# Optimization experiments

Measured on AMD Instinct MI355X. Metric: run time of the kernel, lower is better.

Reference implementation:

```python
import jax, jax.numpy as jnp
import numpy as np

NU = 200000   # num user nodes
NI = 200000   # num item nodes
E = 500000    # edges per relation
D = 128       # in_feats
H = 128       # h_feats
NEG_SLOPE = 0.01  # F.leaky_relu default


def _sage(x_src, x_dst, src, dst, n_dst, W_self, W_neigh, b):
    # DGL SAGEConv('mean'): fc_self(x_dst) + fc_neigh(mean of in-neighbors) + bias
    msg = x_src[src]                                   # [E, d] gather
    agg = jax.ops.segment_sum(msg, dst, num_segments=n_dst)   # [n_dst, d]
    deg = jax.ops.segment_sum(jnp.ones((src.shape[0],), x_src.dtype), dst,
                              num_segments=n_dst)      # [n_dst]
    mean = agg / jnp.maximum(deg, 1.0)[:, None]        # zero in-degree -> 0
    return x_dst @ W_self + mean @ W_neigh + b


def setup_inputs() -> dict:
    key = jax.random.key(0)
    ks = jax.random.split(key, 20)
    s = 1.0 / np.sqrt(D)
    inp = {
        'x_user': jax.random.normal(ks[0], (NU, D), jnp.float32),
        'x_item': jax.random.normal(ks[1], (NI, D), jnp.float32),
        'w1_self_uc': jax.random.normal(ks[2], (D, H), jnp.float32) * s,
        'w1_neigh_uc': jax.random.normal(ks[3], (D, H), jnp.float32) * s,
        'b1_uc': jnp.zeros((H,), jnp.float32),
        'w1_self_iu': jax.random.normal(ks[4], (D, H), jnp.float32) * s,
        'w1_neigh_iu': jax.random.normal(ks[5], (D, H), jnp.float32) * s,
        'b1_iu': jnp.zeros((H,), jnp.float32),
        'w2_self_uc': jax.random.normal(ks[6], (H, H), jnp.float32) * s,
        'w2_neigh_uc': jax.random.normal(ks[7], (H, H), jnp.float32) * s,
        'b2_uc': jnp.zeros((H,), jnp.float32),
        'w2_self_iu': jax.random.normal(ks[8], (H, H), jnp.float32) * s,
        'w2_neigh_iu': jax.random.normal(ks[9], (H, H), jnp.float32) * s,
        'b2_iu': jnp.zeros((H,), jnp.float32),
        'src_uc': jax.random.randint(ks[10], (E,), 0, NU, jnp.int32),
        'dst_uc': jax.random.randint(ks[11], (E,), 0, NI, jnp.int32),
        'src_iu': jax.random.randint(ks[12], (E,), 0, NI, jnp.int32),
        'dst_iu': jax.random.randint(ks[13], (E,), 0, NU, jnp.int32),
    }
    return inp


def reference(x_user, x_item,
              w1_self_uc, w1_neigh_uc, b1_uc, w1_self_iu, w1_neigh_iu, b1_iu,
              w2_self_uc, w2_neigh_uc, b2_uc, w2_self_iu, w2_neigh_iu, b2_iu,
              src_uc, dst_uc, src_iu, dst_iu):
    # layer 1: relation 'clicks' user->item, relation 'clicked_by' item->user
    h1_item = _sage(x_user, x_item, src_uc, dst_uc, NI, w1_self_uc, w1_neigh_uc, b1_uc)
    h1_user = _sage(x_item, x_user, src_iu, dst_iu, NU, w1_self_iu, w1_neigh_iu, b1_iu)
    h1_item = jax.nn.leaky_relu(h1_item, NEG_SLOPE)
    h1_user = jax.nn.leaky_relu(h1_user, NEG_SLOPE)
    # layer 2
    h2_item = _sage(h1_user, h1_item, src_uc, dst_uc, NI, w2_self_uc, w2_neigh_uc, b2_uc)
    h2_user = _sage(h1_item, h1_user, src_iu, dst_iu, NU, w2_self_iu, w2_neigh_iu, b2_iu)
    # stack [user, item] (same shape) for a single output tensor
    return jnp.stack([h2_user, h2_item], axis=0)  # [2, 200000, 128]
```

## Files before the change

### kernel.cpp

```cpp
#include <hip/hip_runtime.h>
#include <hip/hip_bf16.h>

#define D_ 128

typedef __attribute__((ext_vector_type(8))) short s8b;
typedef __attribute__((ext_vector_type(4))) float f4;

union U4 { uint u[4]; s8b v; uint4 q; };

__device__ __forceinline__ void gl16(const void* g, void* lds) {
    __builtin_amdgcn_global_load_lds(
        (const __attribute__((address_space(1))) void*)g,
        (__attribute__((address_space(3))) void*)lds, 16, 0, 0);
}

__device__ __forceinline__ void split2(float f0, float f1, uint& hp, uint& lp) {
    uint u0 = __float_as_uint(f0), u1 = __float_as_uint(f1);
    hp = (u0 >> 16) | (u1 & 0xffff0000u);
    float r0 = f0 - __uint_as_float(u0 & 0xffff0000u);
    float r1 = f1 - __uint_as_float(u1 & 0xffff0000u);
    uint v0 = __float_as_uint(r0), v1 = __float_as_uint(r1);
    uint l0 = (v0 + 0x7fffu + ((v0 >> 16) & 1u)) >> 16;
    uint l1 = (v1 + 0x7fffu + ((v1 >> 16) & 1u)) >> 16;
    lp = l0 | (l1 << 16);
}

__device__ __forceinline__ float4 asf4(uint4 u) {
    return make_float4(__uint_as_float(u.x), __uint_as_float(u.y),
                       __uint_as_float(u.z), __uint_as_float(u.w));
}

__global__ void deg2_kernel(const int* __restrict__ dstA, const int* __restrict__ dstB,
                            int* __restrict__ degA, int* __restrict__ degB, int E) {
    int e = blockIdx.x * blockDim.x + threadIdx.x;
    const int* dst = blockIdx.y ? dstB : dstA;
    int* deg = blockIdx.y ? degB : degA;
    if (e < E) atomicAdd(&deg[dst[e]], 1);
}

__global__ __launch_bounds__(256)
void scan1m(const int* __restrict__ degA, const int* __restrict__ degB,
            int* __restrict__ rpA, int* __restrict__ rpB,
            int* __restrict__ partA, int* __restrict__ partB, int N) {
    const int* deg = blockIdx.y ? degB : degA;
    int* rp = blockIdx.y ? rpB : rpA;
    int* partials = blockIdx.y ? partB : partA;
    int tid = threadIdx.x;
    int i = blockIdx.x * 256 + tid;
    int v = (i < N) ? deg[i] : 0;
    int lane = tid & 63, wid = tid >> 6;
    int x = v;
#pragma unroll
    for (int off = 1; off < 64; off <<= 1) {
        int y = __shfl_up(x, off, 64);
        if (lane >= off) x += y;
    }
    __shared__ int wsum[5];
    if (lane == 63) wsum[wid] = x;
    __syncthreads();
    if (tid == 0) {
        int a = wsum[0], b = wsum[1], c = wsum[2], d = wsum[3];
        wsum[0] = 0; wsum[1] = a; wsum[2] = a + b; wsum[3] = a + b + c;
        wsum[4] = a + b + c + d;
    }
    __syncthreads();
    if (i < N) rp[i] = wsum[wid] + x - v;
    if (tid == 0) partials[blockIdx.x] = wsum[4];
}

__global__ __launch_bounds__(1024)
void scan2m(int* __restrict__ partA, int* __restrict__ partB, int B) {
    int* partials = blockIdx.x ? partB : partA;
    __shared__ int buf[1024];
    int t = threadIdx.x;
    int v = (t < B) ? partials[t] : 0;
    buf[t] = v;
    __syncthreads();
    for (int off = 1; off < 1024; off <<= 1) {
        int add = (t >= off) ? buf[t - off] : 0;
        __syncthreads();
        buf[t] += add;
        __syncthreads();
    }
    if (t < B) partials[t] = buf[t] - v;
}

__global__ __launch_bounds__(256)
void scan3m(int* __restrict__ rpA, int* __restrict__ rpB,
            const int* __restrict__ partA, const int* __restrict__ partB, int N, int E) {
    int* rp = blockIdx.y ? rpB : rpA;
    const int* partials = blockIdx.y ? partB : partA;
    int i = blockIdx.x * 256 + threadIdx.x;
    if (i < N) rp[i] += partials[blockIdx.x];
    if (i == 0) rp[N] = E;
}

__global__ void fill2_csr(const int* __restrict__ srcA, const int* __restrict__ dstA,
                          const int* __restrict__ rpA, int* __restrict__ curA,
                          int* __restrict__ colA, int* __restrict__ colpA,
                          const int* __restrict__ srcB, const int* __restrict__ dstB,
                          const int* __restrict__ rpB, int* __restrict__ curB,
                          int* __restrict__ colB, int* __restrict__ colpB, int E) {
    int e = blockIdx.x * blockDim.x + threadIdx.x;
    if (e >= E) return;
    const int* src = blockIdx.y ? srcB : srcA;
    const int* dst = blockIdx.y ? dstB : dstA;
    const int* rp  = blockIdx.y ? rpB : rpA;
    int* cursor = blockIdx.y ? curB : curA;
    int* col    = blockIdx.y ? colB : colA;
    int* colp   = blockIdx.y ? colpB : colpA;
    int d = dst[e];
    int s = src[e];
    int idx = atomicAdd(&cursor[d], 1);
    col[rp[d] + idx] = s;
    if (idx < 4) colp[d * 4 + idx] = s;
}

__global__ __launch_bounds__(256)
void prep_weights(const float* __restrict__ s0, const float* __restrict__ n0,
                  const float* __restrict__ s1, const float* __restrict__ n1,
                  const float* __restrict__ s2, const float* __restrict__ n2,
                  const float* __restrict__ s3, const float* __restrict__ n3,
                  ushort* __restrict__ WTH, ushort* __restrict__ WTL) {
    int g = blockIdx.y;
    int t = blockIdx.x * 256 + threadIdx.x;
    int c = t & 127;
    int oct = t >> 7;
    const float* self  = g == 0 ? s0 : g == 1 ? s1 : g == 2 ? s2 : s3;
    const float* neigh = g == 0 ? n0 : g == 1 ? n1 : g == 2 ? n2 : n3;
    uint hd[4], ld_[4];
#pragma unroll
    for (int p = 0; p < 4; ++p) {
        uint hpair = 0, lpair = 0;
#pragma unroll
        for (int q = 0; q < 2; ++q) {
            int kv = oct * 8 + p * 2 + q;
            const float* Wsrc = kv < 128 ? self : neigh;
            float f = Wsrc[(size_t)(kv & 127) * 128 + c];
            uint u = __float_as_uint(f);
            uint h = u >> 16;
            float r = f - __uint_as_float(u & 0xffff0000u);
            uint v = __float_as_uint(r);
            uint l = (v + 0x7fffu + ((v >> 16) & 1u)) >> 16;
            hpair |= h << (16 * q);
            lpair |= l << (16 * q);
        }
        hd[p] = hpair; ld_[p] = lpair;
    }
    size_t base = ((size_t)g * 128 + c) * 256 + oct * 8;
    *(uint4*)(WTH + base) = make_uint4(hd[0], hd[1], hd[2], hd[3]);
    *(uint4*)(WTL + base) = make_uint4(ld_[0], ld_[1], ld_[2], ld_[3]);
}

#define AGGH 0
#define AGGL 8192
#define ASTEP 16384
#define WHO 20480
#define WLO 28672

template<int FP32IN, int SPLIT, int LRELU>
__device__ __forceinline__ void fused_body(const char* A1, const char* XN,
        const int* rp, const int* col, const int* colp,
        const ushort* WTh, const ushort* WTl, const float* bias, void* outp,
        int bid, char* smem) {
    const int t = threadIdx.x;
    const int row0 = bid * 32;
    const int li = t & 15;

#pragma unroll
    for (int p = 0; p < 2; ++p) {
        int nl = p * 16 + (t >> 4);
        int node = row0 + nl;
        int beg = rp[node], end = rp[node + 1];
        int dg = end - beg;
        int4 c4 = *(const int4*)(colp + (size_t)node * 4);
        int s0 = dg > 0 ? c4.x : 0;
        int s1 = dg > 1 ? c4.y : 0;
        int s2 = dg > 2 ? c4.z : 0;
        int s3 = dg > 3 ? c4.w : 0;
        float w0 = dg > 0 ? 1.f : 0.f;
        float w1 = dg > 1 ? 1.f : 0.f;
        float w2 = dg > 2 ? 1.f : 0.f;
        float w3 = dg > 3 ? 1.f : 0.f;
        float a[8];
#pragma unroll
        for (int j = 0; j < 8; ++j) a[j] = 0.f;
        const int lo = FP32IN ? li * 32 : li * 16;
        const int d2 = FP32IN ? 16 : 256;
        const char* p0 = XN + (size_t)s0 * 512 + lo;
        const char* p1 = XN + (size_t)s1 * 512 + lo;
        const char* p2 = XN + (size_t)s2 * 512 + lo;
        const char* p3 = XN + (size_t)s3 * 512 + lo;
        uint4 H0 = *(const uint4*)p0, L0 = *(const uint4*)(p0 + d2);
        uint4 H1 = *(const uint4*)p1, L1 = *(const uint4*)(p1 + d2);
        uint4 H2 = *(const uint4*)p2, L2 = *(const uint4*)(p2 + d2);
        uint4 H3 = *(const uint4*)p3, L3 = *(const uint4*)(p3 + d2);
        if (FP32IN) {
#pragma unroll
            for (int q = 0; q < 4; ++q) {
                uint4 Hq = q == 0 ? H0 : q == 1 ? H1 : q == 2 ? H2 : H3;
                uint4 Lq = q == 0 ? L0 : q == 1 ? L1 : q == 2 ? L2 : L3;
                float wq = q == 0 ? w0 : q == 1 ? w1 : q == 2 ? w2 : w3;
                float4 X = asf4(Hq), Y = asf4(Lq);
                a[0] = fmaf(X.x, wq, a[0]); a[1] = fmaf(X.y, wq, a[1]);
                a[2] = fmaf(X.z, wq, a[2]); a[3] = fmaf(X.w, wq, a[3]);
                a[4] = fmaf(Y.x, wq, a[4]); a[5] = fmaf(Y.y, wq, a[5]);
                a[6] = fmaf(Y.z, wq, a[6]); a[7] = fmaf(Y.w, wq, a[7]);
            }
            for (int e = beg + 4; e < end; ++e) {
                const char* pp = XN + (size_t)col[e] * 512 + li * 32;
                float4 X = *(const float4*)pp, Y = *(const float4*)(pp + 16);
                a[0] += X.x; a[1] += X.y; a[2] += X.z; a[3] += X.w;
                a[4] += Y.x; a[5] += Y.y; a[6] += Y.z; a[7] += Y.w;
            }
        } else {
#pragma unroll
            for (int q = 0; q < 4; ++q) {
                uint4 Hq = q == 0 ? H0 : q == 1 ? H1 : q == 2 ? H2 : H3;
                uint4 Lq = q == 0 ? L0 : q == 1 ? L1 : q == 2 ? L2 : L3;
                float wq = q == 0 ? w0 : q == 1 ? w1 : q == 2 ? w2 : w3;
                const ushort* hu = (const ushort*)&Hq;
                const ushort* lu = (const ushort*)&Lq;
#pragma unroll
                for (int j = 0; j < 8; ++j) {
                    float v = __uint_as_float((uint)hu[j] << 16)
                            + __uint_as_float((uint)lu[j] << 16);
                    a[j] = fmaf(v, wq, a[j]);
                }
            }
            for (int e = beg + 4; e < end; ++e) {
                const char* pp = XN + (size_t)col[e] * 512 + li * 16;
                uint4 H = *(const uint4*)pp, L = *(const uint4*)(pp + 256);
                const ushort* hu = (const ushort*)&H;
                const ushort* lu = (const ushort*)&L;
#pragma unroll
                for (int j = 0; j < 8; ++j)
                    a[j] += __uint_as_float((uint)hu[j] << 16)
                          + __uint_as_float((uint)lu[j] << 16);
            }
        }
        float inv = 1.f / (float)(dg > 0 ? dg : 1);
        uint h[4], l[4];
        split2(a[0] * inv, a[1] * inv, h[0], l[0]);
        split2(a[2] * inv, a[3] * inv, h[1], l[1]);
        split2(a[4] * inv, a[5] * inv, h[2], l[2]);
        split2(a[6] * inv, a[7] * inv, h[3], l[3]);
        int chunk = li ^ (nl & 3) ^ (((nl >> 2) & 3) << 2);
        *(uint4*)(smem + AGGH + nl * 256 + chunk * 16) = make_uint4(h[0], h[1], h[2], h[3]);
        *(uint4*)(smem + AGGL + nl * 256 + chunk * 16) = make_uint4(l[0], l[1], l[2], l[3]);
    }

    const int w = t >> 6, lane = t & 63;
    const int fr = lane & 15, hi = lane >> 4;
    const int ncol0 = w * 32;

    f4 acc[2][2];
    {
        float bv[2];
#pragma unroll
        for (int n = 0; n < 2; ++n) bv[n] = bias[ncol0 + n * 16 + fr];
#pragma unroll
        for (int m = 0; m < 2; ++m)
#pragma unroll
            for (int n = 0; n < 2; ++n) acc[m][n] = (f4){bv[n], bv[n], bv[n], bv[n]};
    }

    auto stage = [&](int ks) {
        if (ks < 4) {
            if (FP32IN) {
                int row = t >> 3, cs = t & 7;
                gl16(A1 + (size_t)(row0 + row) * 512 + ks * 128 + ((cs ^ (row & 7)) * 16),
                     smem + ASTEP + t * 16);
            } else {
                int j = t & 127, part = t >> 7;
                int row = j >> 2, cs = j & 3;
                gl16(A1 + (size_t)(row0 + row) * 512 + part * 256 + ks * 64
                         + ((cs ^ ((row >> 1) & 3)) * 16),
                     smem + ASTEP + part * 2048 + j * 16);
            }
        }
#pragma unroll
        for (int it = 0; it < 2; ++it) {
            int j = it * 256 + t;
            int col_ = j >> 2, cs = j & 3;
            size_t so = (size_t)col_ * 512 + ks * 64 + ((cs ^ ((col_ >> 1) & 3)) * 16);
            gl16((const char*)WTh + so, smem + WHO + j * 16);
            gl16((const char*)WTl + so, smem + WLO + j * 16);
        }
    };

    auto compute = [&](int ks) {
        s8b ah[2], al[2], wh[2], wl[2];
        if (ks < 4) {
            if (FP32IN) {
#pragma unroll
                for (int m = 0; m < 2; ++m) {
                    int r = m * 16 + fr;
                    f4 x0 = *(const f4*)(smem + ASTEP + r * 128 + (((hi * 2) ^ (r & 7)) * 16));
                    f4 x1 = *(const f4*)(smem + ASTEP + r * 128 + (((hi * 2 + 1) ^ (r & 7)) * 16));
                    U4 H, L;
                    split2(x0[0], x0[1], H.u[0], L.u[0]);
                    split2(x0[2], x0[3], H.u[1], L.u[1]);
                    split2(x1[0], x1[1], H.u[2], L.u[2]);
                    split2(x1[2], x1[3], H.u[3], L.u[3]);
                    ah[m] = H.v; al[m] = L.v;
                }
            } else {
#pragma unroll
                for (int m = 0; m < 2; ++m) {
                    int r = m * 16 + fr;
                    int off = r * 64 + ((hi ^ ((r >> 1) & 3)) * 16);
                    ah[m] = *(const s8b*)(smem + ASTEP + off);
                    al[m] = *(const s8b*)(smem + ASTEP + 2048 + off);
                }
            }
        } else {
            int kk = ks - 4;
#pragma unroll
            for (int m = 0; m < 2; ++m) {
                int r = m * 16 + fr;
                int chunk = (kk * 4 + hi) ^ (r & 3) ^ (((r >> 2) & 3) << 2);
                ah[m] = *(const s8b*)(smem + AGGH + r * 256 + chunk * 16);
                al[m] = *(const s8b*)(smem + AGGL + r * 256 + chunk * 16);
            }
        }
#pragma unroll
        for (int n = 0; n < 2; ++n) {
            int c = ncol0 + n * 16 + fr;
            int off = c * 64 + ((hi ^ ((c >> 1) & 3)) * 16);
            wh[n] = *(const s8b*)(smem + WHO + off);
            wl[n] = *(const s8b*)(smem + WLO + off);
        }
#pragma unroll
        for (int n = 0; n < 2; ++n)
#pragma unroll
            for (int m = 0; m < 2; ++m) {
                acc[m][n] = __builtin_amdgcn_mfma_f32_16x16x32_bf16(ah[m], wh[n], acc[m][n], 0, 0, 0);
                acc[m][n] = __builtin_amdgcn_mfma_f32_16x16x32_bf16(al[m], wh[n], acc[m][n], 0, 0, 0);
                acc[m][n] = __builtin_amdgcn_mfma_f32_16x16x32_bf16(ah[m], wl[n], acc[m][n], 0, 0, 0);
            }
    };

    for (int ks = 0; ks < 8; ++ks) {
        stage(ks);
        __syncthreads();
        compute(ks);
        __syncthreads();
    }

    float* T = (float*)smem;
#pragma unroll
    for (int m = 0; m < 2; ++m)
#pragma unroll
        for (int n = 0; n < 2; ++n)
#pragma unroll
            for (int r = 0; r < 4; ++r)
                T[(m * 16 + hi * 4 + r) * 132 + ncol0 + n * 16 + fr] = acc[m][n][r];
    __syncthreads();
    {
        int row = t >> 3, q = t & 7;
        int gr = row0 + row;
        if (SPLIT) {
            char* ob = (char*)outp + (size_t)gr * 512;
#pragma unroll
            for (int i = 0; i < 2; ++i) {
                const float* p = T + row * 132 + (q * 2 + i) * 8;
                f4 x0 = *(const f4*)p;
                f4 x1 = *(const f4*)(p + 4);
                float e[8] = {x0[0], x0[1], x0[2], x0[3], x1[0], x1[1], x1[2], x1[3]};
                if (LRELU) {
#pragma unroll
                    for (int j = 0; j < 8; ++j) e[j] = e[j] > 0.f ? e[j] : 0.01f * e[j];
                }
                uint h[4], l[4];
#pragma unroll
                for (int j = 0; j < 4; ++j) split2(e[2 * j], e[2 * j + 1], h[j], l[j]);
                *(uint4*)(ob + (q * 2 + i) * 16) = make_uint4(h[0], h[1], h[2], h[3]);
                *(uint4*)(ob + 256 + (q * 2 + i) * 16) = make_uint4(l[0], l[1], l[2], l[3]);
            }
        } else {
            float* ob = (float*)outp + (size_t)gr * 128;
#pragma unroll
            for (int i = 0; i < 4; ++i) {
                f4 x = *(const f4*)(T + row * 132 + q * 16 + i * 4);
                float e0 = x[0], e1 = x[1], e2 = x[2], e3 = x[3];
                if (LRELU) {
                    e0 = e0 > 0.f ? e0 : 0.01f * e0;
                    e1 = e1 > 0.f ? e1 : 0.01f * e1;
                    e2 = e2 > 0.f ? e2 : 0.01f * e2;
                    e3 = e3 > 0.f ? e3 : 0.01f * e3;
                }
                *(float4*)(ob + q * 16 + i * 4) = make_float4(e0, e1, e2, e3);
            }
        }
    }
}

template<int FP32IN, int SPLIT, int LRELU>
__global__ __launch_bounds__(256, 4)
void fused2k(const void* A1a, const void* XNa, const int* rpA, const int* colA,
             const int* colpA, const ushort* WTha, const ushort* WTla,
             const float* ba, void* outa,
             const void* A1b, const void* XNb, const int* rpB, const int* colB,
             const int* colpB, const ushort* WThb, const ushort* WTlb,
             const float* bb, void* outb, int blocksA) {
    __shared__ __align__(16) char smem[36864];
    bool isA = (int)blockIdx.x < blocksA;
    int bid = isA ? blockIdx.x : blockIdx.x - blocksA;
    if (isA)
        fused_body<FP32IN, SPLIT, LRELU>((const char*)A1a, (const char*)XNa, rpA, colA,
                                         colpA, WTha, WTla, ba, outa, bid, smem);
    else
        fused_body<FP32IN, SPLIT, LRELU>((const char*)A1b, (const char*)XNb, rpB, colB,
                                         colpB, WThb, WTlb, bb, outb, bid, smem);
}

extern "C" void kernel_launch(void* const* d_in, const int* in_sizes, int n_in,
                              void* d_out, int out_size, void* d_ws, size_t ws_size,
                              hipStream_t stream) {
    const float* x_user     = (const float*)d_in[0];
    const float* x_item     = (const float*)d_in[1];
    const float* w1_self_uc = (const float*)d_in[2];
    const float* w1_neigh_uc= (const float*)d_in[3];
    const float* b1_uc      = (const float*)d_in[4];
    const float* w1_self_iu = (const float*)d_in[5];
    const float* w1_neigh_iu= (const float*)d_in[6];
    const float* b1_iu      = (const float*)d_in[7];
    const float* w2_self_uc = (const float*)d_in[8];
    const float* w2_neigh_uc= (const float*)d_in[9];
    const float* b2_uc      = (const float*)d_in[10];
    const float* w2_self_iu = (const float*)d_in[11];
    const float* w2_neigh_iu= (const float*)d_in[12];
    const float* b2_iu      = (const float*)d_in[13];
    const int* src_uc = (const int*)d_in[14];
    const int* dst_uc = (const int*)d_in[15];
    const int* src_iu = (const int*)d_in[16];
    const int* dst_iu = (const int*)d_in[17];

    const int NU = in_sizes[0] / D_;
    const int NI = in_sizes[1] / D_;
    const int E  = in_sizes[14];

    float* f_user = (float*)d_out;
    float* f_item = (float*)d_out + (size_t)NU * 128;

    char* ws = (char*)d_ws;
    const size_t FEAT_BYTES = (size_t)200000 * 512;
    char* h1_item  = ws;          ws += FEAT_BYTES;
    char* h1_user  = ws;          ws += FEAT_BYTES;
    ushort* WTH    = (ushort*)ws; ws += (size_t)4 * 128 * 256 * sizeof(ushort);
    ushort* WTL    = (ushort*)ws; ws += (size_t)4 * 128 * 256 * sizeof(ushort);
    int* colp_uc   = (int*)ws;    ws += (size_t)200000 * 4 * sizeof(int);
    int* colp_iu   = (int*)ws;    ws += (size_t)200000 * 4 * sizeof(int);
    int* rp_uc     = (int*)ws;    ws += (size_t)(NI + 1) * sizeof(int);
    int* rp_iu     = (int*)ws;    ws += (size_t)(NU + 1) * sizeof(int);
    int* col_uc    = (int*)ws;    ws += (size_t)E * sizeof(int);
    int* col_iu    = (int*)ws;    ws += (size_t)E * sizeof(int);
    int* deg_uc    = (int*)ws;    ws += (size_t)200000 * sizeof(int);
    int* deg_iu    = (int*)ws;    ws += (size_t)200000 * sizeof(int);
    int* cur_uc    = (int*)ws;    ws += (size_t)200000 * sizeof(int);
    int* cur_iu    = (int*)ws;    ws += (size_t)200000 * sizeof(int);
    int* partA     = (int*)ws;    ws += (size_t)1024 * sizeof(int);
    int* partB     = (int*)ws;    ws += (size_t)1024 * sizeof(int);

    const int TPB = 256;
    const int eBlocks  = (E + TPB - 1) / TPB;
    const int sBlocks  = (200000 + 255) / 256;
    const int mBlocksI = (NI + 31) / 32;
    const int mBlocksU = (NU + 31) / 32;
    const size_t WSTRIDE = (size_t)128 * 256;

    hipMemsetAsync(deg_uc, 0, (size_t)4 * 200000 * sizeof(int), stream);

    prep_weights<<<dim3(16, 4), 256, 0, stream>>>(
        w1_self_uc, w1_neigh_uc, w1_self_iu, w1_neigh_iu,
        w2_self_uc, w2_neigh_uc, w2_self_iu, w2_neigh_iu, WTH, WTL);

    deg2_kernel<<<dim3(eBlocks, 2), TPB, 0, stream>>>(dst_uc, dst_iu, deg_uc, deg_iu, E);
    scan1m<<<dim3(sBlocks, 2), 256, 0, stream>>>(deg_uc, deg_iu, rp_uc, rp_iu, partA, partB, 200000);
    scan2m<<<2, 1024, 0, stream>>>(partA, partB, sBlocks);
    scan3m<<<dim3(sBlocks, 2), 256, 0, stream>>>(rp_uc, rp_iu, partA, partB, 200000, E);
    fill2_csr<<<dim3(eBlocks, 2), TPB, 0, stream>>>(src_uc, dst_uc, rp_uc, cur_uc, col_uc, colp_uc,
                                                    src_iu, dst_iu, rp_iu, cur_iu, col_iu, colp_iu, E);

    fused2k<1, 1, 1><<<mBlocksI + mBlocksU, 256, 0, stream>>>(
        x_item, x_user, rp_uc, col_uc, colp_uc, WTH + 0 * WSTRIDE, WTL + 0 * WSTRIDE,
        b1_uc, h1_item,
        x_user, x_item, rp_iu, col_iu, colp_iu, WTH + 1 * WSTRIDE, WTL + 1 * WSTRIDE,
        b1_iu, h1_user, mBlocksI);

    fused2k<0, 0, 0><<<mBlocksI + mBlocksU, 256, 0, stream>>>(
        h1_item, h1_user, rp_uc, col_uc, colp_uc, WTH + 2 * WSTRIDE, WTL + 2 * WSTRIDE,
        b2_uc, f_item,
        h1_user, h1_item, rp_iu, col_iu, colp_iu, WTH + 3 * WSTRIDE, WTL + 3 * WSTRIDE,
        b2_iu, f_user, mBlocksI);
}
```

Measured before the change: 628.8 us.

## Double row tile to 64 with 512 threads, wider K stages, 8-neighbor prefetch

The fused SAGE kernel now processes 64 destination rows per block with 512 threads. Waves split the output tile over both rows and columns, so each staged weight slice is reused across twice as many rows. The K loop runs in 4 wider phases of 64 instead of 8 phases of 32, which halves the number of barriers. The CSR prefix cache grows from 4 to 8 neighbors, so up to 8 neighbor loads are issued together before the serial col[] loop. In exchange, shared memory rises to 80KB per block, which may limit occupancy, and the prefix array uses twice the memory.

```diff
diff --git a/kernel.cpp b/kernel.cpp
--- a/kernel.cpp
+++ b/kernel.cpp
@@ -113,7 +113,7 @@
     int s = src[e];
     int idx = atomicAdd(&cursor[d], 1);
     col[rp[d] + idx] = s;
-    if (idx < 4) colp[d * 4 + idx] = s;
+    if (idx < 8) colp[(size_t)d * 8 + idx] = s;
 }
 
 __global__ __launch_bounds__(256)
@@ -153,10 +153,10 @@
 }
 
 #define AGGH 0
-#define AGGL 8192
-#define ASTEP 16384
-#define WHO 20480
-#define WLO 28672
+#define AGGL 16384
+#define ASTEP 32768
+#define WHO 49152
+#define WLO 65536
 
 template<int FP32IN, int SPLIT, int LRELU>
 __device__ __forceinline__ void fused_body(const char* A1, const char* XN,
@@ -164,16 +164,16 @@
         const ushort* WTh, const ushort* WTl, const float* bias, void* outp,
         int bid, char* smem) {
     const int t = threadIdx.x;
-    const int row0 = bid * 32;
+    const int row0 = bid * 64;
     const int li = t & 15;
 
 #pragma unroll
     for (int p = 0; p < 2; ++p) {
-        int nl = p * 16 + (t >> 4);
+        int nl = p * 32 + (t >> 4);
         int node = row0 + nl;
         int beg = rp[node], end = rp[node + 1];
         int dg = end - beg;
-        int4 c4 = *(const int4*)(colp + (size_t)node * 4);
+        int4 c4 = *(const int4*)(colp + (size_t)node * 8);
         int s0 = dg > 0 ? c4.x : 0;
         int s1 = dg > 1 ? c4.y : 0;
         int s2 = dg > 2 ? c4.z : 0;
@@ -187,56 +187,92 @@
         for (int j = 0; j < 8; ++j) a[j] = 0.f;
         const int lo = FP32IN ? li * 32 : li * 16;
         const int d2 = FP32IN ? 16 : 256;
-        const char* p0 = XN + (size_t)s0 * 512 + lo;
-        const char* p1 = XN + (size_t)s1 * 512 + lo;
-        const char* p2 = XN + (size_t)s2 * 512 + lo;
-        const char* p3 = XN + (size_t)s3 * 512 + lo;
-        uint4 H0 = *(const uint4*)p0, L0 = *(const uint4*)(p0 + d2);
-        uint4 H1 = *(const uint4*)p1, L1 = *(const uint4*)(p1 + d2);
-        uint4 H2 = *(const uint4*)p2, L2 = *(const uint4*)(p2 + d2);
-        uint4 H3 = *(const uint4*)p3, L3 = *(const uint4*)(p3 + d2);
-        if (FP32IN) {
+        {
+            const char* p0 = XN + (size_t)s0 * 512 + lo;
+            const char* p1 = XN + (size_t)s1 * 512 + lo;
+            const char* p2 = XN + (size_t)s2 * 512 + lo;
+            const char* p3 = XN + (size_t)s3 * 512 + lo;
+            uint4 H0 = *(const uint4*)p0, L0 = *(const uint4*)(p0 + d2);
+            uint4 H1 = *(const uint4*)p1, L1 = *(const uint4*)(p1 + d2);
+            uint4 H2 = *(const uint4*)p2, L2 = *(const uint4*)(p2 + d2);
+            uint4 H3 = *(const uint4*)p3, L3 = *(const uint4*)(p3 + d2);
 #pragma unroll
             for (int q = 0; q < 4; ++q) {
                 uint4 Hq = q == 0 ? H0 : q == 1 ? H1 : q == 2 ? H2 : H3;
                 uint4 Lq = q == 0 ? L0 : q == 1 ? L1 : q == 2 ? L2 : L3;
                 float wq = q == 0 ? w0 : q == 1 ? w1 : q == 2 ? w2 : w3;
-                float4 X = asf4(Hq), Y = asf4(Lq);
-                a[0] = fmaf(X.x, wq, a[0]); a[1] = fmaf(X.y, wq, a[1]);
-                a[2] = fmaf(X.z, wq, a[2]); a[3] = fmaf(X.w, wq, a[3]);
-                a[4] = fmaf(Y.x, wq, a[4]); a[5] = fmaf(Y.y, wq, a[5]);
-                a[6] = fmaf(Y.z, wq, a[6]); a[7] = fmaf(Y.w, wq, a[7]);
-            }
-            for (int e = beg + 4; e < end; ++e) {
-                const char* pp = XN + (size_t)col[e] * 512 + li * 32;
-                float4 X = *(const float4*)pp, Y = *(const float4*)(pp + 16);
-                a[0] += X.x; a[1] += X.y; a[2] += X.z; a[3] += X.w;
-                a[4] += Y.x; a[5] += Y.y; a[6] += Y.z; a[7] += Y.w;
-            }
-        } else {
+                if (FP32IN) {
+                    float4 X = asf4(Hq), Y = asf4(Lq);
+                    a[0] = fmaf(X.x, wq, a[0]); a[1] = fmaf(X.y, wq, a[1]);
+                    a[2] = fmaf(X.z, wq, a[2]); a[3] = fmaf(X.w, wq, a[3]);
+                    a[4] = fmaf(Y.x, wq, a[4]); a[5] = fmaf(Y.y, wq, a[5]);
+                    a[6] = fmaf(Y.z, wq, a[6]); a[7] = fmaf(Y.w, wq, a[7]);
+                } else {
+                    const ushort* hu = (const ushort*)&Hq;
+                    const ushort* lu = (const ushort*)&Lq;
+#pragma unroll
+                    for (int j = 0; j < 8; ++j) {
+                        float v = __uint_as_float((uint)hu[j] << 16)
+                                + __uint_as_float((uint)lu[j] << 16);
+                        a[j] = fmaf(v, wq, a[j]);
+                    }
+                }
+            }
+        }
+        if (dg > 4) {
+            int4 c4b = *(const int4*)(colp + (size_t)node * 8 + 4);
+            int s4 = c4b.x;
+            int s5 = dg > 5 ? c4b.y : s4;
+            int s6 = dg > 6 ? c4b.z : s4;
+            int s7 = dg > 7 ? c4b.w : s4;
+            float w5 = dg > 5 ? 1.f : 0.f;
+            float w6 = dg > 6 ? 1.f : 0.f;
+            float w7 = dg > 7 ? 1.f : 0.f;
+            const char* p4 = XN + (size_t)s4 * 512 + lo;
+            const char* p5 = XN + (size_t)s5 * 512 + lo;
+            const char* p6 = XN + (size_t)s6 * 512 + lo;
+            const char* p7 = XN + (size_t)s7 * 512 + lo;
+            uint4 H4 = *(const uint4*)p4, L4 = *(const uint4*)(p4 + d2);
+            uint4 H5 = *(const uint4*)p5, L5 = *(const uint4*)(p5 + d2);
+            uint4 H6 = *(const uint4*)p6, L6 = *(const uint4*)(p6 + d2);
+            uint4 H7 = *(const uint4*)p7, L7 = *(const uint4*)(p7 + d2);
 #pragma unroll
             for (int q = 0; q < 4; ++q) {
-                uint4 Hq = q == 0 ? H0 : q == 1 ? H1 : q == 2 ? H2 : H3;
-                uint4 Lq = q == 0 ? L0 : q == 1 ? L1 : q == 2 ? L2 : L3;
-                float wq = q == 0 ? w0 : q == 1 ? w1 : q == 2 ? w2 : w3;
-                const ushort* hu = (const ushort*)&Hq;
-                const ushort* lu = (const ushort*)&Lq;
-#pragma unroll
-                for (int j = 0; j < 8; ++j) {
-                    float v = __uint_as_float((uint)hu[j] << 16)
-                            + __uint_as_float((uint)lu[j] << 16);
-                    a[j] = fmaf(v, wq, a[j]);
-                }
-            }
-            for (int e = beg + 4; e < end; ++e) {
-                const char* pp = XN + (size_t)col[e] * 512 + li * 16;
-                uint4 H = *(const uint4*)pp, L = *(const uint4*)(pp + 256);
-                const ushort* hu = (const ushort*)&H;
-                const ushort* lu = (const ushort*)&L;
-#pragma unroll
-                for (int j = 0; j < 8; ++j)
-                    a[j] += __uint_as_float((uint)hu[j] << 16)
-                          + __uint_as_float((uint)lu[j] << 16);
+                uint4 Hq = q == 0 ? H4 : q == 1 ? H5 : q == 2 ? H6 : H7;
+                uint4 Lq = q == 0 ? L4 : q == 1 ? L5 : q == 2 ? L6 : L7;
+                float wq = q == 0 ? 1.f : q == 1 ? w5 : q == 2 ? w6 : w7;
+                if (FP32IN) {
+                    float4 X = asf4(Hq), Y = asf4(Lq);
+                    a[0] = fmaf(X.x, wq, a[0]); a[1] = fmaf(X.y, wq, a[1]);
+                    a[2] = fmaf(X.z, wq, a[2]); a[3] = fmaf(X.w, wq, a[3]);
+                    a[4] = fmaf(Y.x, wq, a[4]); a[5] = fmaf(Y.y, wq, a[5]);
+                    a[6] = fmaf(Y.z, wq, a[6]); a[7] = fmaf(Y.w, wq, a[7]);
+                } else {
+                    const ushort* hu = (const ushort*)&Hq;
+                    const ushort* lu = (const ushort*)&Lq;
+#pragma unroll
+                    for (int j = 0; j < 8; ++j) {
+                        float v = __uint_as_float((uint)hu[j] << 16)
+                                + __uint_as_float((uint)lu[j] << 16);
+                        a[j] = fmaf(v, wq, a[j]);
+                    }
+                }
+            }
+            for (int e = beg + 8; e < end; ++e) {
+                const char* pp = XN + (size_t)col[e] * 512 + lo;
+                uint4 H = *(const uint4*)pp, L = *(const uint4*)(pp + d2);
+                if (FP32IN) {
+                    float4 X = asf4(H), Y = asf4(L);
+                    a[0] += X.x; a[1] += X.y; a[2] += X.z; a[3] += X.w;
+                    a[4] += Y.x; a[5] += Y.y; a[6] += Y.z; a[7] += Y.w;
+                } else {
+                    const ushort* hu = (const ushort*)&H;
+                    const ushort* lu = (const ushort*)&L;
+#pragma unroll
+                    for (int j = 0; j < 8; ++j)
+                        a[j] += __uint_as_float((uint)hu[j] << 16)
+                              + __uint_as_float((uint)lu[j] << 16);
+                }
             }
         }
         float inv = 1.f / (float)(dg > 0 ? dg : 1);
@@ -252,7 +288,7 @@
 
     const int w = t >> 6, lane = t & 63;
     const int fr = lane & 15, hi = lane >> 4;
-    const int ncol0 = w * 32;
+    const int mrow0 = (w & 1) * 32, ncol0 = (w >> 1) * 32;
 
     f4 acc[2][2];
     {
@@ -265,97 +301,99 @@
             for (int n = 0; n < 2; ++n) acc[m][n] = (f4){bv[n], bv[n], bv[n], bv[n]};
     }
 
-    auto stage = [&](int ks) {
-        if (ks < 4) {
+    for (int ph = 0; ph < 4; ++ph) {
+        if (ph < 2) {
             if (FP32IN) {
-                int row = t >> 3, cs = t & 7;
-                gl16(A1 + (size_t)(row0 + row) * 512 + ks * 128 + ((cs ^ (row & 7)) * 16),
-                     smem + ASTEP + t * 16);
+#pragma unroll
+                for (int it = 0; it < 2; ++it) {
+                    int j = it * 512 + t;
+                    int row = j >> 4, c = j & 15;
+                    gl16(A1 + (size_t)(row0 + row) * 512 + ph * 256
+                             + ((c ^ ((row & 7) << 1)) * 16),
+                         smem + ASTEP + j * 16);
+                }
             } else {
-                int j = t & 127, part = t >> 7;
-                int row = j >> 2, cs = j & 3;
-                gl16(A1 + (size_t)(row0 + row) * 512 + part * 256 + ks * 64
-                         + ((cs ^ ((row >> 1) & 3)) * 16),
-                     smem + ASTEP + part * 2048 + j * 16);
+                int j = t;
+                int row = j >> 3, c2 = j & 7;
+                size_t so = (size_t)(row0 + row) * 512 + ph * 128 + ((c2 ^ (row & 7)) * 16);
+                gl16(A1 + so, smem + ASTEP + j * 16);
+                gl16(A1 + so + 256, smem + ASTEP + 8192 + j * 16);
             }
         }
 #pragma unroll
         for (int it = 0; it < 2; ++it) {
-            int j = it * 256 + t;
-            int col_ = j >> 2, cs = j & 3;
-            size_t so = (size_t)col_ * 512 + ks * 64 + ((cs ^ ((col_ >> 1) & 3)) * 16);
+            int j = it * 512 + t;
+            int col_ = j >> 3, c2 = j & 7;
+            size_t so = (size_t)col_ * 512 + ph * 128 + ((c2 ^ (col_ & 7)) * 16);
             gl16((const char*)WTh + so, smem + WHO + j * 16);
             gl16((const char*)WTl + so, smem + WLO + j * 16);
         }
-    };
-
-    auto compute = [&](int ks) {
-        s8b ah[2], al[2], wh[2], wl[2];
-        if (ks < 4) {
-            if (FP32IN) {
+        __syncthreads();
+
+#pragma unroll
+        for (int j = 0; j < 2; ++j) {
+            s8b ah[2], al[2], wh[2], wl[2];
+            if (ph < 2) {
+                if (FP32IN) {
+#pragma unroll
+                    for (int m = 0; m < 2; ++m) {
+                        int r = mrow0 + m * 16 + fr;
+                        int c0 = ((j * 8 + hi * 2) ^ ((r & 7) << 1));
+                        f4 x0 = *(const f4*)(smem + ASTEP + r * 256 + c0 * 16);
+                        f4 x1 = *(const f4*)(smem + ASTEP + r * 256 + c0 * 16 + 16);
+                        U4 H, L;
+                        split2(x0[0], x0[1], H.u[0], L.u[0]);
+                        split2(x0[2], x0[3], H.u[1], L.u[1]);
+                        split2(x1[0], x1[1], H.u[2], L.u[2]);
+                        split2(x1[2], x1[3], H.u[3], L.u[3]);
+                        ah[m] = H.v; al[m] = L.v;
+                    }
+                } else {
+#pragma unroll
+                    for (int m = 0; m < 2; ++m) {
+                        int r = mrow0 + m * 16 + fr;
+                        int chunk = (j * 4 + hi) ^ (r & 7);
+                        ah[m] = *(const s8b*)(smem + ASTEP + r * 128 + chunk * 16);
+                        al[m] = *(const s8b*)(smem + ASTEP + 8192 + r * 128 + chunk * 16);
+                    }
+                }
+            } else {
+                int kk = (ph - 2) * 2 + j;
 #pragma unroll
                 for (int m = 0; m < 2; ++m) {
-                    int r = m * 16 + fr;
-                    f4 x0 = *(const f4*)(smem + ASTEP + r * 128 + (((hi * 2) ^ (r & 7)) * 16));
-                    f4 x1 = *(const f4*)(smem + ASTEP + r * 128 + (((hi * 2 + 1) ^ (r & 7)) * 16));
-                    U4 H, L;
-                    split2(x0[0], x0[1], H.u[0], L.u[0]);
-                    split2(x0[2], x0[3], H.u[1], L.u[1]);
-                    split2(x1[0], x1[1], H.u[2], L.u[2]);
-                    split2(x1[2], x1[3], H.u[3], L.u[3]);
-                    ah[m] = H.v; al[m] = L.v;
-                }
-            } else {
+                    int r = mrow0 + m * 16 + fr;
+                    int chunk = (kk * 4 + hi) ^ (r & 3) ^ (((r >> 2) & 3) << 2);
+                    ah[m] = *(const s8b*)(smem + AGGH + r * 256 + chunk * 16);
+                    al[m] = *(const s8b*)(smem + AGGL + r * 256 + chunk * 16);
+                }
+            }
+#pragma unroll
+            for (int n = 0; n < 2; ++n) {
+                int c = ncol0 + n * 16 + fr;
+                int chunk = (j * 4 + hi) ^ (c & 7);
+                wh[n] = *(const s8b*)(smem + WHO + c * 128 + chunk * 16);
+                wl[n] = *(const s8b*)(smem + WLO + c * 128 + chunk * 16);
+            }
+#pragma unroll
+            for (int n = 0; n < 2; ++n)
 #pragma unroll
                 for (int m = 0; m < 2; ++m) {
-                    int r = m * 16 + fr;
-                    int off = r * 64 + ((hi ^ ((r >> 1) & 3)) * 16);
-                    ah[m] = *(const s8b*)(smem + ASTEP + off);
-                    al[m] = *(const s8b*)(smem + ASTEP + 2048 + off);
-                }
-            }
-        } else {
-            int kk = ks - 4;
-#pragma unroll
-            for (int m = 0; m < 2; ++m) {
-                int r = m * 16 + fr;
-                int chunk = (kk * 4 + hi) ^ (r & 3) ^ (((r >> 2) & 3) << 2);
-                ah[m] = *(const s8b*)(smem + AGGH + r * 256 + chunk * 16);
-                al[m] = *(const s8b*)(smem + AGGL + r * 256 + chunk * 16);
-            }
-        }
-#pragma unroll
-        for (int n = 0; n < 2; ++n) {
-            int c = ncol0 + n * 16 + fr;
-            int off = c * 64 + ((hi ^ ((c >> 1) & 3)) * 16);
-            wh[n] = *(const s8b*)(smem + WHO + off);
-            wl[n] = *(const s8b*)(smem + WLO + off);
-        }
+                    acc[m][n] = __builtin_amdgcn_mfma_f32_16x16x32_bf16(ah[m], wh[n], acc[m][n], 0, 0, 0);
+                    acc[m][n] = __builtin_amdgcn_mfma_f32_16x16x32_bf16(al[m], wh[n], acc[m][n], 0, 0, 0);
+                    acc[m][n] = __builtin_amdgcn_mfma_f32_16x16x32_bf16(ah[m], wl[n], acc[m][n], 0, 0, 0);
+                }
+        }
+        __syncthreads();
+    }
+
+    float* T = (float*)smem;
+#pragma unroll
+    for (int m = 0; m < 2; ++m)
 #pragma unroll
         for (int n = 0; n < 2; ++n)
 #pragma unroll
-            for (int m = 0; m < 2; ++m) {
-                acc[m][n] = __builtin_amdgcn_mfma_f32_16x16x32_bf16(ah[m], wh[n], acc[m][n], 0, 0, 0);
-                acc[m][n] = __builtin_amdgcn_mfma_f32_16x16x32_bf16(al[m], wh[n], acc[m][n], 0, 0, 0);
-                acc[m][n] = __builtin_amdgcn_mfma_f32_16x16x32_bf16(ah[m], wl[n], acc[m][n], 0, 0, 0);
-            }
-    };
-
-    for (int ks = 0; ks < 8; ++ks) {
-        stage(ks);
-        __syncthreads();
-        compute(ks);
-        __syncthreads();
-    }
-
-    float* T = (float*)smem;
-#pragma unroll
-    for (int m = 0; m < 2; ++m)
-#pragma unroll
-        for (int n = 0; n < 2; ++n)
-#pragma unroll
             for (int r = 0; r < 4; ++r)
-                T[(m * 16 + hi * 4 + r) * 132 + ncol0 + n * 16 + fr] = acc[m][n][r];
+                T[(mrow0 + m * 16 + hi * 4 + r) * 132 + ncol0 + n * 16 + fr] = acc[m][n][r];
     __syncthreads();
     {
         int row = t >> 3, q = t & 7;
@@ -370,11 +408,11 @@
                 float e[8] = {x0[0], x0[1], x0[2], x0[3], x1[0], x1[1], x1[2], x1[3]};
                 if (LRELU) {
 #pragma unroll
-                    for (int j = 0; j < 8; ++j) e[j] = e[j] > 0.f ? e[j] : 0.01f * e[j];
+                    for (int jj = 0; jj < 8; ++jj) e[jj] = e[jj] > 0.f ? e[jj] : 0.01f * e[jj];
                 }
                 uint h[4], l[4];
 #pragma unroll
-                for (int j = 0; j < 4; ++j) split2(e[2 * j], e[2 * j + 1], h[j], l[j]);
+                for (int jj = 0; jj < 4; ++jj) split2(e[2 * jj], e[2 * jj + 1], h[jj], l[jj]);
                 *(uint4*)(ob + (q * 2 + i) * 16) = make_uint4(h[0], h[1], h[2], h[3]);
                 *(uint4*)(ob + 256 + (q * 2 + i) * 16) = make_uint4(l[0], l[1], l[2], l[3]);
             }
@@ -397,14 +435,14 @@
 }
 
 template<int FP32IN, int SPLIT, int LRELU>
-__global__ __launch_bounds__(256, 4)
+__global__ __launch_bounds__(512, 4)
 void fused2k(const void* A1a, const void* XNa, const int* rpA, const int* colA,
              const int* colpA, const ushort* WTha, const ushort* WTla,
              const float* ba, void* outa,
              const void* A1b, const void* XNb, const int* rpB, const int* colB,
              const int* colpB, const ushort* WThb, const ushort* WTlb,
              const float* bb, void* outb, int blocksA) {
-    __shared__ __align__(16) char smem[36864];
+    __shared__ __align__(16) char smem[81920];
     bool isA = (int)blockIdx.x < blocksA;
     int bid = isA ? blockIdx.x : blockIdx.x - blocksA;
     if (isA)
@@ -450,8 +488,8 @@
     char* h1_user  = ws;          ws += FEAT_BYTES;
     ushort* WTH    = (ushort*)ws; ws += (size_t)4 * 128 * 256 * sizeof(ushort);
     ushort* WTL    = (ushort*)ws; ws += (size_t)4 * 128 * 256 * sizeof(ushort);
-    int* colp_uc   = (int*)ws;    ws += (size_t)200000 * 4 * sizeof(int);
-    int* colp_iu   = (int*)ws;    ws += (size_t)200000 * 4 * sizeof(int);
+    int* colp_uc   = (int*)ws;    ws += (size_t)200000 * 8 * sizeof(int);
+    int* colp_iu   = (int*)ws;    ws += (size_t)200000 * 8 * sizeof(int);
     int* rp_uc     = (int*)ws;    ws += (size_t)(NI + 1) * sizeof(int);
     int* rp_iu     = (int*)ws;    ws += (size_t)(NU + 1) * sizeof(int);
     int* col_uc    = (int*)ws;    ws += (size_t)E * sizeof(int);
@@ -466,8 +504,8 @@
     const int TPB = 256;
     const int eBlocks  = (E + TPB - 1) / TPB;
     const int sBlocks  = (200000 + 255) / 256;
-    const int mBlocksI = (NI + 31) / 32;
-    const int mBlocksU = (NU + 31) / 32;
+    const int mBlocksI = (NI + 63) / 64;
+    const int mBlocksU = (NU + 63) / 64;
     const size_t WSTRIDE = (size_t)128 * 256;
 
     hipMemsetAsync(deg_uc, 0, (size_t)4 * 200000 * sizeof(int), stream);
@@ -483,13 +521,13 @@
     fill2_csr<<<dim3(eBlocks, 2), TPB, 0, stream>>>(src_uc, dst_uc, rp_uc, cur_uc, col_uc, colp_uc,
                                                     src_iu, dst_iu, rp_iu, cur_iu, col_iu, colp_iu, E);
 
-    fused2k<1, 1, 1><<<mBlocksI + mBlocksU, 256, 0, stream>>>(
+    fused2k<1, 1, 1><<<mBlocksI + mBlocksU, 512, 0, stream>>>(
         x_item, x_user, rp_uc, col_uc, colp_uc, WTH + 0 * WSTRIDE, WTL + 0 * WSTRIDE,
         b1_uc, h1_item,
         x_user, x_item, rp_iu, col_iu, colp_iu, WTH + 1 * WSTRIDE, WTL + 1 * WSTRIDE,
         b1_iu, h1_user, mBlocksI);
 
-    fused2k<0, 0, 0><<<mBlocksI + mBlocksU, 256, 0, stream>>>(
+    fused2k<0, 0, 0><<<mBlocksI + mBlocksU, 512, 0, stream>>>(
         h1_item, h1_user, rp_uc, col_uc, colp_uc, WTH + 2 * WSTRIDE, WTL + 2 * WSTRIDE,
         b2_uc, f_item,
         h1_user, h1_item, rp_iu, col_iu, colp_iu, WTH + 3 * WSTRIDE, WTL + 3 * WSTRIDE,
```

Result: faster. 529.8 us (median of 2 runs) (-15.8%).
